# Performance work log

Hardware: AMD Instinct MI355X
Metric: run time of the kernel (lower is better)

The kernel has to match this reference:

```python
import jax, jax.numpy as jnp
import numpy as np

ALPHA = 0.2  # leaky relu slope
NEG = -9e15  # mask fill value from the torch code


def gat_layer(x, adj_mask, W, a):
    """One dense GAT attention head.
    Equivalent math to the torch layer, without materializing the
    [N, N, 2F] a_input tensor: a^T [h_i ; h_j] = (h @ a1)_i + (h @ a2)_j.
    x: [N, Fin], adj_mask: [N, N] bool, W: [Fin, Fout], a: [2*Fout, 1].
    """
    h = x @ W                              # [N, Fout]
    Fo = W.shape[1]
    s_src = h @ a[:Fo, 0]                  # [N]
    s_dst = h @ a[Fo:, 0]                  # [N]
    e = jax.nn.leaky_relu(s_src[:, None] + s_dst[None, :], ALPHA)  # [N, N]
    e = jnp.where(adj_mask, e, NEG)
    attn = jax.nn.softmax(e, axis=1)       # dropout is a no-op in eval mode
    return attn @ h                        # [N, Fout]


def setup_inputs() -> dict:
    key = jax.random.key(0)
    ks = jax.random.split(key, 6)
    N, nfeat, nhid, nclass, nheads = 4096, 512, 64, 32, 8
    x = jax.random.normal(ks[0], (N, nfeat), dtype=jnp.float32)
    adj = jax.random.randint(ks[1], (N, N), 0, 2, dtype=jnp.int32)
    # params scaled like torch uniform(-1/sqrt(fan_in), 1/sqrt(fan_in))
    W_att = jax.random.normal(ks[2], (nheads, nfeat, nhid), dtype=jnp.float32) / np.sqrt(nfeat)
    a_att = jax.random.normal(ks[3], (nheads, 2 * nhid, 1), dtype=jnp.float32) / np.sqrt(2 * nhid)
    W_out = jax.random.normal(ks[4], (nhid * nheads, nclass), dtype=jnp.float32) / np.sqrt(nhid * nheads)
    a_out = jax.random.normal(ks[5], (2 * nclass, 1), dtype=jnp.float32) / np.sqrt(2 * nclass)
    return {"x": x, "adj": adj, "W_att": W_att, "a_att": a_att,
            "W_out": W_out, "a_out": a_out}


def reference(x, adj, W_att, a_att, W_out, a_out):
    adj_mask = adj > 0  # [N, N]
    # multi-head layer, concat=True => elu per head, concat along features
    heads = jax.vmap(lambda W, a: jax.nn.elu(gat_layer(x, adj_mask, W, a)))(W_att, a_att)  # [H, N, nhid]
    H, N, Fh = heads.shape
    hcat = jnp.transpose(heads, (1, 0, 2)).reshape(N, H * Fh)  # [N, H*nhid]
    # output layer, concat=False, then elu applied by GAT.forward
    out = jax.nn.elu(gat_layer(hcat, adj_mask, W_out, a_out))  # [N, nclass]
    return out
```

## Files before the change

### kernel.cpp

```cpp
#include <hip/hip_runtime.h>
#include <math.h>

#define NN 4096
#define CC 512
#define MB (1024*1024)
#define LOG2E 1.4426950408889634f

typedef __attribute__((ext_vector_type(8))) __bf16 bf16x8;
typedef __attribute__((ext_vector_type(4))) float f32x4;
typedef unsigned short ushort_t;
typedef unsigned int uint_t;
typedef unsigned char uchar_t;

#if __has_builtin(__builtin_amdgcn_exp2f)
#define EXP2(x) __builtin_amdgcn_exp2f(x)
#else
#define EXP2(x) exp2f(x)
#endif

static __device__ __forceinline__ float elu1(float x){ return x > 0.f ? x : (__expf(x)-1.f); }
static __device__ __forceinline__ ushort_t f2bf(float f){
    union { float f; uint_t u; } v; v.f = f;
    uint_t r = (v.u + 0x7FFFu + ((v.u >> 16) & 1u)) >> 16;
    return (ushort_t)r;
}
static __device__ __forceinline__ float bf2f(ushort_t h){
    union { uint_t u; float f; } q; q.u = ((uint_t)h) << 16; return q.f;
}

__global__ void k_prep(const float* __restrict__ Watt, const float* __restrict__ Wout,
                       ushort_t* __restrict__ Wh, ushort_t* __restrict__ Wl,
                       ushort_t* __restrict__ Wth, ushort_t* __restrict__ Wtl){
    int idx = blockIdx.x*256 + threadIdx.x;
    if (idx < 512*128){
        int c = idx >> 7, kq = idx & 127, k = kq*4;
        ushort4 h4, l4;
        float v[4];
        #pragma unroll
        for(int j=0;j<4;j++)
            v[j] = Watt[(c>>6)*(512*64) + (k+j)*64 + (c&63)];
        h4.x = f2bf(v[0]); h4.y = f2bf(v[1]); h4.z = f2bf(v[2]); h4.w = f2bf(v[3]);
        l4.x = f2bf(v[0]-bf2f(h4.x)); l4.y = f2bf(v[1]-bf2f(h4.y));
        l4.z = f2bf(v[2]-bf2f(h4.z)); l4.w = f2bf(v[3]-bf2f(h4.w));
        *(ushort4*)&Wh[(size_t)c*512 + k] = h4;
        *(ushort4*)&Wl[(size_t)c*512 + k] = l4;
    } else if (idx < 512*128 + 32*128){
        int idx2 = idx - 512*128;
        int n = idx2 >> 7, kq = idx2 & 127, k = kq*4;
        ushort4 h4, l4;
        float v[4];
        #pragma unroll
        for(int j=0;j<4;j++)
            v[j] = Wout[(size_t)(k+j)*32 + n];
        h4.x = f2bf(v[0]); h4.y = f2bf(v[1]); h4.z = f2bf(v[2]); h4.w = f2bf(v[3]);
        l4.x = f2bf(v[0]-bf2f(h4.x)); l4.y = f2bf(v[1]-bf2f(h4.y));
        l4.z = f2bf(v[2]-bf2f(h4.z)); l4.w = f2bf(v[3]-bf2f(h4.w));
        *(ushort4*)&Wth[(size_t)n*512 + k] = h4;
        *(ushort4*)&Wtl[(size_t)n*512 + k] = l4;
    }
}

__global__ void k_splitx(const float* __restrict__ x,
                         ushort_t* __restrict__ xh, ushort_t* __restrict__ xl){
    int idx = blockIdx.x*256 + threadIdx.x;
    float4 v = *(const float4*)&x[(size_t)idx*4];
    ushort4 h4, l4;
    h4.x = f2bf(v.x); h4.y = f2bf(v.y); h4.z = f2bf(v.z); h4.w = f2bf(v.w);
    l4.x = f2bf(v.x-bf2f(h4.x)); l4.y = f2bf(v.y-bf2f(h4.y));
    l4.z = f2bf(v.z-bf2f(h4.z)); l4.w = f2bf(v.w-bf2f(h4.w));
    *(ushort4*)&xh[(size_t)idx*4] = h4;
    *(ushort4*)&xl[(size_t)idx*4] = l4;
}

__global__ void k_pack(const int* __restrict__ adj, uint_t* __restrict__ abits){
    int idx = blockIdx.x*256 + threadIdx.x;
    int i = idx >> 7, q = idx & 127;
    const int4* p = (const int4*)&adj[(size_t)i*NN + q*32];
    uint_t m = 0;
    #pragma unroll
    for(int g=0; g<8; g++){
        int4 v = p[g];
        m |= (uint_t)(v.x > 0) << (g*4 + 0);
        m |= (uint_t)(v.y > 0) << (g*4 + 1);
        m |= (uint_t)(v.z > 0) << (g*4 + 2);
        m |= (uint_t)(v.w > 0) << (g*4 + 3);
    }
    abits[idx] = m;
}

__global__ __launch_bounds__(256) void k_gemm1(
        const ushort_t* __restrict__ xh, const ushort_t* __restrict__ xl,
        const ushort_t* __restrict__ Wh, const ushort_t* __restrict__ Wl,
        const float* __restrict__ aatt,
        ushort_t* __restrict__ hT,
        float* __restrict__ ssrc2, float* __restrict__ sdst2){
    const int t = threadIdx.x;
    const int l = t & 63, wv = t >> 6;
    const int lr = l & 15, lg = l >> 4;
    const int ib = blockIdx.x*64 + wv*16;
    const int hd = blockIdx.y;
    const int j0 = hd*64;

    f32x4 acc[4] = {};
    #pragma unroll 2
    for(int ks=0; ks<16; ks++){
        const int kb = ks*32 + lg*8;
        bf16x8 ah = *(const bf16x8*)&xh[(size_t)(ib+lr)*512 + kb];
        bf16x8 al = *(const bf16x8*)&xl[(size_t)(ib+lr)*512 + kb];
        bf16x8 bh[4], bl[4];
        #pragma unroll
        for(int nt=0;nt<4;nt++){
            bh[nt] = *(const bf16x8*)&Wh[(size_t)(j0+nt*16+lr)*512 + kb];
            bl[nt] = *(const bf16x8*)&Wl[(size_t)(j0+nt*16+lr)*512 + kb];
        }
        #pragma unroll
        for(int nt=0;nt<4;nt++){
            acc[nt] = __builtin_amdgcn_mfma_f32_16x16x32_bf16(ah, bh[nt], acc[nt], 0,0,0);
            acc[nt] = __builtin_amdgcn_mfma_f32_16x16x32_bf16(al, bh[nt], acc[nt], 0,0,0);
            acc[nt] = __builtin_amdgcn_mfma_f32_16x16x32_bf16(ah, bl[nt], acc[nt], 0,0,0);
        }
    }
    #pragma unroll
    for(int nt=0;nt<4;nt++){
        const int col = j0 + nt*16 + lr;
        ushort4 o;
        o.x = f2bf(acc[nt][0]); o.y = f2bf(acc[nt][1]);
        o.z = f2bf(acc[nt][2]); o.w = f2bf(acc[nt][3]);
        *(ushort4*)&hT[(size_t)col*NN + ib + lg*4] = o;
    }
    float a1v[4], a2v[4];
    #pragma unroll
    for(int nt=0;nt<4;nt++){
        a1v[nt] = aatt[hd*128 + nt*16 + lr];
        a2v[nt] = aatt[hd*128 + 64 + nt*16 + lr];
    }
    #pragma unroll
    for(int r=0;r<4;r++){
        float ps = acc[0][r]*a1v[0] + acc[1][r]*a1v[1] + acc[2][r]*a1v[2] + acc[3][r]*a1v[3];
        float pd = acc[0][r]*a2v[0] + acc[1][r]*a2v[1] + acc[2][r]*a2v[2] + acc[3][r]*a2v[3];
        #pragma unroll
        for(int m=1;m<16;m<<=1){
            ps += __shfl_xor(ps, m);
            pd += __shfl_xor(pd, m);
        }
        if (lr == 0){
            ssrc2[hd*NN + ib + lg*4 + r] = ps*LOG2E;
            sdst2[hd*NN + ib + lg*4 + r] = pd*LOG2E;
        }
    }
}

__global__ __launch_bounds__(512, 2) void k_attn1(
        const ushort_t* __restrict__ hT,
        const float* __restrict__ ssrc2, const float* __restrict__ sdst2,
        const uchar_t* __restrict__ abits,
        ushort_t* __restrict__ hch, ushort_t* __restrict__ hcl){
    const int t = threadIdx.x;
    const int l = t & 63, wv = t >> 6;
    const int hd = blockIdx.y;
    const int i0 = blockIdx.x*64;
    const int lr = l & 15, lg = l >> 4;

    f32x4 acc[4][4] = {};
    f32x4 dacc[4] = {};

    float ss[4];
    #pragma unroll
    for(int mh=0;mh<4;mh++)
        ss[mh] = ssrc2[hd*NN + i0 + mh*16 + lr];

    bf16x8 ones;
    #pragma unroll
    for(int e=0;e<8;e++) ones[e] = (__bf16)1.0f;

    const int jwb = wv*512;
    const uchar_t* arow[4];
    #pragma unroll
    for(int mh=0;mh<4;mh++)
        arow[mh] = &abits[(size_t)(i0 + mh*16 + lr)*512 + (jwb >> 3)];

    bf16x8 bA[4], bB[4];
    float4 sdaA, sdbA, sdaB, sdbB;
    uint_t bitsA[4], bitsB[4];

#define LOAD1(SFX, JT) { \
    const int jb_ = jwb + (JT)*32 + lg*8; \
    _Pragma("unroll") \
    for(int nt=0;nt<4;nt++) \
        b##SFX[nt] = *(const bf16x8*)&hT[(size_t)(hd*64 + nt*16 + lr)*NN + jb_]; \
    sda##SFX = *(const float4*)&sdst2[hd*NN + jb_]; \
    sdb##SFX = *(const float4*)&sdst2[hd*NN + jb_ + 4]; \
    _Pragma("unroll") \
    for(int mh=0;mh<4;mh++) \
        bits##SFX[mh] = arow[mh][(JT)*4 + lg]; }

#define COMP1(SFX) { \
    float sdv[8] = {sda##SFX.x, sda##SFX.y, sda##SFX.z, sda##SFX.w, \
                    sdb##SFX.x, sdb##SFX.y, sdb##SFX.z, sdb##SFX.w}; \
    _Pragma("unroll") \
    for(int mh=0;mh<4;mh++){ \
        const uint_t bits = bits##SFX[mh]; \
        bf16x8 a; \
        _Pragma("unroll") \
        for(int e=0;e<8;e++){ \
            float s_ = ss[mh] + sdv[e]; \
            float t_ = fmaxf(s_, 0.2f*s_); \
            float w_ = EXP2(t_) * (float)((bits >> e) & 1u); \
            a[e] = (__bf16)w_; \
        } \
        _Pragma("unroll") \
        for(int nt=0;nt<4;nt++) \
            acc[mh][nt] = __builtin_amdgcn_mfma_f32_16x16x32_bf16( \
                a, b##SFX[nt], acc[mh][nt], 0, 0, 0); \
        dacc[mh] = __builtin_amdgcn_mfma_f32_16x16x32_bf16( \
                a, ones, dacc[mh], 0, 0, 0); \
    } }

    LOAD1(A, 0);
    for(int jt=0; jt<16; jt+=2){
        LOAD1(B, jt+1);
        COMP1(A);
        if (jt + 2 < 16) LOAD1(A, jt+2);
        COMP1(B);
    }
#undef LOAD1
#undef COMP1

    __shared__ f32x4 red[4][10][64];

#define CHUNK_REDUCE(M0) { \
    __syncthreads(); \
    if (wv >= 4){ \
        _Pragma("unroll") \
        for(int m=0;m<2;m++){ \
            _Pragma("unroll") \
            for(int nt=0;nt<4;nt++) red[wv-4][m*4+nt][l] = acc[(M0)+m][nt]; \
            red[wv-4][8+m][l] = dacc[(M0)+m]; \
        } \
    } \
    __syncthreads(); \
    if (wv < 4){ \
        _Pragma("unroll") \
        for(int m=0;m<2;m++){ \
            _Pragma("unroll") \
            for(int nt=0;nt<4;nt++) acc[(M0)+m][nt] += red[wv][m*4+nt][l]; \
            dacc[(M0)+m] += red[wv][8+m][l]; \
        } \
    } \
    __syncthreads(); \
    if (wv == 2 || wv == 3){ \
        _Pragma("unroll") \
        for(int m=0;m<2;m++){ \
            _Pragma("unroll") \
            for(int nt=0;nt<4;nt++) red[wv-2][m*4+nt][l] = acc[(M0)+m][nt]; \
            red[wv-2][8+m][l] = dacc[(M0)+m]; \
        } \
    } \
    __syncthreads(); \
    if (wv < 2){ \
        _Pragma("unroll") \
        for(int m=0;m<2;m++){ \
            _Pragma("unroll") \
            for(int nt=0;nt<4;nt++) acc[(M0)+m][nt] += red[wv][m*4+nt][l]; \
            dacc[(M0)+m] += red[wv][8+m][l]; \
        } \
    } \
    __syncthreads(); \
    if (wv == 1){ \
        _Pragma("unroll") \
        for(int m=0;m<2;m++){ \
            _Pragma("unroll") \
            for(int nt=0;nt<4;nt++) red[0][m*4+nt][l] = acc[(M0)+m][nt]; \
            red[0][8+m][l] = dacc[(M0)+m]; \
        } \
    } \
    __syncthreads(); \
    if (wv == 0){ \
        _Pragma("unroll") \
        for(int m=0;m<2;m++){ \
            const int mh = (M0)+m; \
            _Pragma("unroll") \
            for(int nt=0;nt<4;nt++) acc[mh][nt] += red[0][m*4+nt][l]; \
            dacc[mh] += red[0][8+m][l]; \
            _Pragma("unroll") \
            for(int nt=0;nt<4;nt++){ \
                const int col = hd*64 + nt*16 + lr; \
                _Pragma("unroll") \
                for(int r=0;r<4;r++){ \
                    const int row = i0 + mh*16 + lg*4 + r; \
                    float v_ = elu1(acc[mh][nt][r] / dacc[mh][r]); \
                    ushort_t hi_ = f2bf(v_); \
                    hch[(size_t)row*512 + col] = hi_; \
                    hcl[(size_t)row*512 + col] = f2bf(v_ - bf2f(hi_)); \
                } \
            } \
        } \
    } }

    CHUNK_REDUCE(0);
    CHUNK_REDUCE(2);
#undef CHUNK_REDUCE
}

__global__ __launch_bounds__(256) void k_gemm2(
        const ushort_t* __restrict__ hch, const ushort_t* __restrict__ hcl,
        const ushort_t* __restrict__ Wth, const ushort_t* __restrict__ Wtl,
        const float* __restrict__ aout,
        ushort_t* __restrict__ h2T, float* __restrict__ ss2, float* __restrict__ sd2){
    const int t = threadIdx.x;
    const int l = t & 63, wv = t >> 6;
    const int lr = l & 15, lg = l >> 4;
    const int ib = blockIdx.x*64 + wv*16;

    f32x4 acc[2] = {};
    #pragma unroll 2
    for(int ks=0; ks<16; ks++){
        const int kb = ks*32 + lg*8;
        bf16x8 ah = *(const bf16x8*)&hch[(size_t)(ib+lr)*512 + kb];
        bf16x8 al = *(const bf16x8*)&hcl[(size_t)(ib+lr)*512 + kb];
        bf16x8 bh[2], bl[2];
        #pragma unroll
        for(int nt=0;nt<2;nt++){
            bh[nt] = *(const bf16x8*)&Wth[(size_t)(nt*16+lr)*512 + kb];
            bl[nt] = *(const bf16x8*)&Wtl[(size_t)(nt*16+lr)*512 + kb];
        }
        #pragma unroll
        for(int nt=0;nt<2;nt++){
            acc[nt] = __builtin_amdgcn_mfma_f32_16x16x32_bf16(ah, bh[nt], acc[nt], 0,0,0);
            acc[nt] = __builtin_amdgcn_mfma_f32_16x16x32_bf16(al, bh[nt], acc[nt], 0,0,0);
            acc[nt] = __builtin_amdgcn_mfma_f32_16x16x32_bf16(ah, bl[nt], acc[nt], 0,0,0);
        }
    }
    #pragma unroll
    for(int nt=0;nt<2;nt++)
        #pragma unroll
        for(int r=0;r<4;r++)
            h2T[(size_t)(nt*16+lr)*NN + ib + lg*4 + r] = f2bf(acc[nt][r]);
    float a1v[2], a2v[2];
    #pragma unroll
    for(int nt=0;nt<2;nt++){
        a1v[nt] = aout[nt*16 + lr];
        a2v[nt] = aout[32 + nt*16 + lr];
    }
    #pragma unroll
    for(int r=0;r<4;r++){
        float ps = acc[0][r]*a1v[0] + acc[1][r]*a1v[1];
        float pd = acc[0][r]*a2v[0] + acc[1][r]*a2v[1];
        #pragma unroll
        for(int m=1;m<16;m<<=1){
            ps += __shfl_xor(ps, m);
            pd += __shfl_xor(pd, m);
        }
        if (lr == 0){
            ss2[ib + lg*4 + r] = ps*LOG2E;
            sd2[ib + lg*4 + r] = pd*LOG2E;
        }
    }
}

__global__ __launch_bounds__(256) void k_attn2(
        const ushort_t* __restrict__ h2T,
        const float* __restrict__ ss2, const float* __restrict__ sd2,
        const uchar_t* __restrict__ abits,
        float* __restrict__ pnum2T, float* __restrict__ pden2){
    const int t = threadIdx.x;
    const int l = t & 63, wv = t >> 6;
    const int i0 = blockIdx.x*64;
    const int jc = blockIdx.y;
    const int lr = l & 15, lg = l >> 4;

    f32x4 acc[4][2] = {};
    f32x4 dacc[4] = {};

    float ss[4];
    #pragma unroll
    for(int mh=0;mh<4;mh++)
        ss[mh] = ss2[i0 + mh*16 + lr];

    bf16x8 ones;
    #pragma unroll
    for(int e=0;e<8;e++) ones[e] = (__bf16)1.0f;

    const int jwb = jc*512 + wv*128;
    const uchar_t* arow[4];
    #pragma unroll
    for(int mh=0;mh<4;mh++)
        arow[mh] = &abits[(size_t)(i0 + mh*16 + lr)*512 + (jwb >> 3)];

    bf16x8 bA[2], bB[2];
    float4 sdaA, sdbA, sdaB, sdbB;
    uint_t bitsA[4], bitsB[4];

#define LOAD2(SFX, JT) { \
    const int jb_ = jwb + (JT)*32 + lg*8; \
    _Pragma("unroll") \
    for(int nt=0;nt<2;nt++) \
        b##SFX[nt] = *(const bf16x8*)&h2T[(size_t)(nt*16 + lr)*NN + jb_]; \
    sda##SFX = *(const float4*)&sd2[jb_]; \
    sdb##SFX = *(const float4*)&sd2[jb_ + 4]; \
    _Pragma("unroll") \
    for(int mh=0;mh<4;mh++) \
        bits##SFX[mh] = arow[mh][(JT)*4 + lg]; }

#define COMP2(SFX) { \
    float sdv[8] = {sda##SFX.x, sda##SFX.y, sda##SFX.z, sda##SFX.w, \
                    sdb##SFX.x, sdb##SFX.y, sdb##SFX.z, sdb##SFX.w}; \
    _Pragma("unroll") \
    for(int mh=0;mh<4;mh++){ \
        const uint_t bits = bits##SFX[mh]; \
        bf16x8 a; \
        _Pragma("unroll") \
        for(int e=0;e<8;e++){ \
            float s_ = ss[mh] + sdv[e]; \
            float t_ = fmaxf(s_, 0.2f*s_); \
            float w_ = EXP2(t_) * (float)((bits >> e) & 1u); \
            a[e] = (__bf16)w_; \
        } \
        _Pragma("unroll") \
        for(int nt=0;nt<2;nt++) \
            acc[mh][nt] = __builtin_amdgcn_mfma_f32_16x16x32_bf16( \
                a, b##SFX[nt], acc[mh][nt], 0, 0, 0); \
        dacc[mh] = __builtin_amdgcn_mfma_f32_16x16x32_bf16( \
                a, ones, dacc[mh], 0, 0, 0); \
    } }

    LOAD2(A, 0);
    for(int jt=0; jt<4; jt+=2){
        LOAD2(B, jt+1);
        COMP2(A);
        if (jt + 2 < 4) LOAD2(A, jt+2);
        COMP2(B);
    }
#undef LOAD2
#undef COMP2

    __shared__ f32x4 red2[2][12][64];
    __syncthreads();
    if (wv >= 2){
        #pragma unroll
        for(int mh=0;mh<4;mh++){
            #pragma unroll
            for(int nt=0;nt<2;nt++) red2[wv-2][mh*2+nt][l] = acc[mh][nt];
            red2[wv-2][8+mh][l] = dacc[mh];
        }
    }
    __syncthreads();
    if (wv < 2){
        #pragma unroll
        for(int mh=0;mh<4;mh++){
            #pragma unroll
            for(int nt=0;nt<2;nt++) acc[mh][nt] += red2[wv][mh*2+nt][l];
            dacc[mh] += red2[wv][8+mh][l];
        }
    }
    __syncthreads();
    if (wv == 1){
        #pragma unroll
        for(int mh=0;mh<4;mh++){
            #pragma unroll
            for(int nt=0;nt<2;nt++) red2[0][mh*2+nt][l] = acc[mh][nt];
            red2[0][8+mh][l] = dacc[mh];
        }
    }
    __syncthreads();
    if (wv == 0){
        #pragma unroll
        for(int mh=0;mh<4;mh++){
            #pragma unroll
            for(int nt=0;nt<2;nt++){
                f32x4 v = acc[mh][nt] + red2[0][mh*2+nt][l];
                int col = nt*16 + lr;
                float4 o = {v[0], v[1], v[2], v[3]};
                *(float4*)&pnum2T[((size_t)jc*32 + col)*NN + i0 + mh*16 + lg*4] = o;
            }
            f32x4 d = dacc[mh] + red2[0][8+mh][l];
            if (lr == 0){
                #pragma unroll
                for(int r=0;r<4;r++)
                    pden2[(size_t)jc*NN + i0 + mh*16 + lg*4 + r] = d[r];
            }
        }
    }
}

__global__ void k_reduce2(const float* __restrict__ pnum2T, const float* __restrict__ pden2,
                          float* __restrict__ out){
    int idx = blockIdx.x*256 + threadIdx.x;
    int c = idx >> 10, i4 = (idx & 1023)*4;
    f32x4 s = {}, d = {};
    #pragma unroll
    for(int jc=0;jc<8;jc++){
        s += *(const f32x4*)&pnum2T[((size_t)jc*32 + c)*NN + i4];
        d += *(const f32x4*)&pden2[(size_t)jc*NN + i4];
    }
    #pragma unroll
    for(int r=0;r<4;r++)
        out[(size_t)(i4+r)*32 + c] = elu1(s[r]/d[r]);
}

extern "C" void kernel_launch(void* const* d_in, const int* in_sizes, int n_in,
                              void* d_out, int out_size, void* d_ws, size_t ws_size,
                              hipStream_t stream){
    const float* x    = (const float*)d_in[0];
    const int*   adj  = (const int*)  d_in[1];
    const float* Watt = (const float*)d_in[2];
    const float* aatt = (const float*)d_in[3];
    const float* Wout = (const float*)d_in[4];
    const float* aout = (const float*)d_in[5];
    float* out = (float*)d_out;
    char* ws = (char*)d_ws;

    ushort_t* hch   = (ushort_t*)(ws + (size_t) 0*MB);
    ushort_t* hcl   = (ushort_t*)(ws + (size_t) 4*MB);
    ushort_t* Whi   = (ushort_t*)(ws + (size_t) 8*MB);
    ushort_t* Wlo   = (ushort_t*)(ws + (size_t) 8*MB + 512*1024);
    float*    ssrc2 = (float*)   (ws + (size_t) 9*MB);
    float*    sdst2 = (float*)   (ws + (size_t)10*MB);
    ushort_t* hT    = (ushort_t*)(ws + (size_t)11*MB);
    uint_t*   abits = (uint_t*)  (ws + (size_t)15*MB);
    ushort_t* Wth   = (ushort_t*)(ws + (size_t)17*MB);
    ushort_t* Wtl   = (ushort_t*)(ws + (size_t)17*MB + 64*1024);
    float*    ss2   = (float*)   (ws + (size_t)18*MB);
    float*    sd2   = (float*)   (ws + (size_t)19*MB);
    ushort_t* h2T   = (ushort_t*)(ws + (size_t)20*MB);
    float*    pden2 = (float*)   (ws + (size_t)21*MB);
    float*    pnum2T= (float*)   (ws + (size_t)22*MB);
    ushort_t* xh    = (ushort_t*)(ws + (size_t)26*MB);
    ushort_t* xl    = (ushort_t*)(ws + (size_t)30*MB);
    if (ws_size < (size_t)40*MB) return;

    k_prep    <<<272, 256, 0, stream>>>(Watt, Wout, Whi, Wlo, Wth, Wtl);
    k_splitx  <<<2048, 256, 0, stream>>>(x, xh, xl);
    k_pack    <<<2048, 256, 0, stream>>>(adj, abits);
    k_gemm1   <<<dim3(64,8), 256, 0, stream>>>(xh, xl, Whi, Wlo, aatt, hT, ssrc2, sdst2);
    k_attn1   <<<dim3(64,8), 512, 0, stream>>>(hT, ssrc2, sdst2, (const uchar_t*)abits, hch, hcl);
    k_gemm2   <<<64, 256, 0, stream>>>(hch, hcl, Wth, Wtl, aout, h2T, ss2, sd2);
    k_attn2   <<<dim3(64,8), 256, 0, stream>>>(h2T, ss2, sd2, (const uchar_t*)abits, pnum2T, pden2);
    k_reduce2 <<<128, 256, 0, stream>>>(pnum2T, pden2, out);
}
```

Before: 257.8 us.

## Merge prep kernels into one launch and retile attention to 32-row blocks

The three preprocessing kernels (weight split, x split, adjacency bit packing) become a single launch that dispatches on block index, removing two kernel launches. The first-layer attention kernel moves from 64-row, 8-wave blocks to 32-row, 4-wave blocks over twice as many blocks. Each wave now covers 1024 columns instead of 512 and holds half the accumulators. The multi-stage shared-memory tree reduction becomes a single store, one barrier, and a four-way sum. This trades register pressure and reduction barriers for more blocks, and each block now reloads its hT tiles for only 32 rows.

```diff
diff --git a/kernel.cpp b/kernel.cpp
--- a/kernel.cpp
+++ b/kernel.cpp
@@ -28,64 +28,65 @@
     union { uint_t u; float f; } q; q.u = ((uint_t)h) << 16; return q.f;
 }
 
-__global__ void k_prep(const float* __restrict__ Watt, const float* __restrict__ Wout,
-                       ushort_t* __restrict__ Wh, ushort_t* __restrict__ Wl,
-                       ushort_t* __restrict__ Wth, ushort_t* __restrict__ Wtl){
-    int idx = blockIdx.x*256 + threadIdx.x;
-    if (idx < 512*128){
-        int c = idx >> 7, kq = idx & 127, k = kq*4;
+__global__ void k_prepare(const float* __restrict__ x, const int* __restrict__ adj,
+                          const float* __restrict__ Watt, const float* __restrict__ Wout,
+                          ushort_t* __restrict__ xh, ushort_t* __restrict__ xl,
+                          uint_t* __restrict__ abits,
+                          ushort_t* __restrict__ Wh, ushort_t* __restrict__ Wl,
+                          ushort_t* __restrict__ Wth, ushort_t* __restrict__ Wtl){
+    const int bid = blockIdx.x;
+    if (bid < 2048){
+        int idx = bid*256 + threadIdx.x;
+        float4 v = *(const float4*)&x[(size_t)idx*4];
         ushort4 h4, l4;
-        float v[4];
-        #pragma unroll
-        for(int j=0;j<4;j++)
-            v[j] = Watt[(c>>6)*(512*64) + (k+j)*64 + (c&63)];
-        h4.x = f2bf(v[0]); h4.y = f2bf(v[1]); h4.z = f2bf(v[2]); h4.w = f2bf(v[3]);
-        l4.x = f2bf(v[0]-bf2f(h4.x)); l4.y = f2bf(v[1]-bf2f(h4.y));
-        l4.z = f2bf(v[2]-bf2f(h4.z)); l4.w = f2bf(v[3]-bf2f(h4.w));
-        *(ushort4*)&Wh[(size_t)c*512 + k] = h4;
-        *(ushort4*)&Wl[(size_t)c*512 + k] = l4;
-    } else if (idx < 512*128 + 32*128){
-        int idx2 = idx - 512*128;
-        int n = idx2 >> 7, kq = idx2 & 127, k = kq*4;
-        ushort4 h4, l4;
-        float v[4];
-        #pragma unroll
-        for(int j=0;j<4;j++)
-            v[j] = Wout[(size_t)(k+j)*32 + n];
-        h4.x = f2bf(v[0]); h4.y = f2bf(v[1]); h4.z = f2bf(v[2]); h4.w = f2bf(v[3]);
-        l4.x = f2bf(v[0]-bf2f(h4.x)); l4.y = f2bf(v[1]-bf2f(h4.y));
-        l4.z = f2bf(v[2]-bf2f(h4.z)); l4.w = f2bf(v[3]-bf2f(h4.w));
-        *(ushort4*)&Wth[(size_t)n*512 + k] = h4;
-        *(ushort4*)&Wtl[(size_t)n*512 + k] = l4;
-    }
-}
-
-__global__ void k_splitx(const float* __restrict__ x,
-                         ushort_t* __restrict__ xh, ushort_t* __restrict__ xl){
-    int idx = blockIdx.x*256 + threadIdx.x;
-    float4 v = *(const float4*)&x[(size_t)idx*4];
-    ushort4 h4, l4;
-    h4.x = f2bf(v.x); h4.y = f2bf(v.y); h4.z = f2bf(v.z); h4.w = f2bf(v.w);
-    l4.x = f2bf(v.x-bf2f(h4.x)); l4.y = f2bf(v.y-bf2f(h4.y));
-    l4.z = f2bf(v.z-bf2f(h4.z)); l4.w = f2bf(v.w-bf2f(h4.w));
-    *(ushort4*)&xh[(size_t)idx*4] = h4;
-    *(ushort4*)&xl[(size_t)idx*4] = l4;
-}
-
-__global__ void k_pack(const int* __restrict__ adj, uint_t* __restrict__ abits){
-    int idx = blockIdx.x*256 + threadIdx.x;
-    int i = idx >> 7, q = idx & 127;
-    const int4* p = (const int4*)&adj[(size_t)i*NN + q*32];
-    uint_t m = 0;
-    #pragma unroll
-    for(int g=0; g<8; g++){
-        int4 v = p[g];
-        m |= (uint_t)(v.x > 0) << (g*4 + 0);
-        m |= (uint_t)(v.y > 0) << (g*4 + 1);
-        m |= (uint_t)(v.z > 0) << (g*4 + 2);
-        m |= (uint_t)(v.w > 0) << (g*4 + 3);
-    }
-    abits[idx] = m;
+        h4.x = f2bf(v.x); h4.y = f2bf(v.y); h4.z = f2bf(v.z); h4.w = f2bf(v.w);
+        l4.x = f2bf(v.x-bf2f(h4.x)); l4.y = f2bf(v.y-bf2f(h4.y));
+        l4.z = f2bf(v.z-bf2f(h4.z)); l4.w = f2bf(v.w-bf2f(h4.w));
+        *(ushort4*)&xh[(size_t)idx*4] = h4;
+        *(ushort4*)&xl[(size_t)idx*4] = l4;
+    } else if (bid < 4096){
+        int idx = (bid-2048)*256 + threadIdx.x;
+        int i = idx >> 7, q = idx & 127;
+        const int4* p = (const int4*)&adj[(size_t)i*NN + q*32];
+        uint_t m = 0;
+        #pragma unroll
+        for(int g=0; g<8; g++){
+            int4 v = p[g];
+            m |= (uint_t)(v.x > 0) << (g*4 + 0);
+            m |= (uint_t)(v.y > 0) << (g*4 + 1);
+            m |= (uint_t)(v.z > 0) << (g*4 + 2);
+            m |= (uint_t)(v.w > 0) << (g*4 + 3);
+        }
+        abits[idx] = m;
+    } else {
+        int idx = (bid-4096)*256 + threadIdx.x;
+        if (idx < 512*128){
+            int c = idx >> 7, k = (idx & 127)*4;
+            ushort4 h4, l4;
+            float v[4];
+            #pragma unroll
+            for(int j=0;j<4;j++)
+                v[j] = Watt[(c>>6)*(512*64) + (k+j)*64 + (c&63)];
+            h4.x = f2bf(v[0]); h4.y = f2bf(v[1]); h4.z = f2bf(v[2]); h4.w = f2bf(v[3]);
+            l4.x = f2bf(v[0]-bf2f(h4.x)); l4.y = f2bf(v[1]-bf2f(h4.y));
+            l4.z = f2bf(v[2]-bf2f(h4.z)); l4.w = f2bf(v[3]-bf2f(h4.w));
+            *(ushort4*)&Wh[(size_t)c*512 + k] = h4;
+            *(ushort4*)&Wl[(size_t)c*512 + k] = l4;
+        } else if (idx < 512*128 + 32*128){
+            int idx2 = idx - 512*128;
+            int n = idx2 >> 7, k = (idx2 & 127)*4;
+            ushort4 h4, l4;
+            float v[4];
+            #pragma unroll
+            for(int j=0;j<4;j++)
+                v[j] = Wout[(size_t)(k+j)*32 + n];
+            h4.x = f2bf(v[0]); h4.y = f2bf(v[1]); h4.z = f2bf(v[2]); h4.w = f2bf(v[3]);
+            l4.x = f2bf(v[0]-bf2f(h4.x)); l4.y = f2bf(v[1]-bf2f(h4.y));
+            l4.z = f2bf(v[2]-bf2f(h4.z)); l4.w = f2bf(v[3]-bf2f(h4.w));
+            *(ushort4*)&Wth[(size_t)n*512 + k] = h4;
+            *(ushort4*)&Wtl[(size_t)n*512 + k] = l4;
+        }
+    }
 }
 
 __global__ __launch_bounds__(256) void k_gemm1(
@@ -150,7 +151,7 @@
     }
 }
 
-__global__ __launch_bounds__(512, 2) void k_attn1(
+__global__ __launch_bounds__(256) void k_attn1(
         const ushort_t* __restrict__ hT,
         const float* __restrict__ ssrc2, const float* __restrict__ sdst2,
         const uchar_t* __restrict__ abits,
@@ -158,30 +159,30 @@
     const int t = threadIdx.x;
     const int l = t & 63, wv = t >> 6;
     const int hd = blockIdx.y;
-    const int i0 = blockIdx.x*64;
+    const int i0 = blockIdx.x*32;
     const int lr = l & 15, lg = l >> 4;
 
-    f32x4 acc[4][4] = {};
-    f32x4 dacc[4] = {};
-
-    float ss[4];
-    #pragma unroll
-    for(int mh=0;mh<4;mh++)
+    f32x4 acc[2][4] = {};
+    f32x4 dacc[2] = {};
+
+    float ss[2];
+    #pragma unroll
+    for(int mh=0;mh<2;mh++)
         ss[mh] = ssrc2[hd*NN + i0 + mh*16 + lr];
 
     bf16x8 ones;
     #pragma unroll
     for(int e=0;e<8;e++) ones[e] = (__bf16)1.0f;
 
-    const int jwb = wv*512;
-    const uchar_t* arow[4];
-    #pragma unroll
-    for(int mh=0;mh<4;mh++)
+    const int jwb = wv*1024;
+    const uchar_t* arow[2];
+    #pragma unroll
+    for(int mh=0;mh<2;mh++)
         arow[mh] = &abits[(size_t)(i0 + mh*16 + lr)*512 + (jwb >> 3)];
 
     bf16x8 bA[4], bB[4];
     float4 sdaA, sdbA, sdaB, sdbB;
-    uint_t bitsA[4], bitsB[4];
+    uint_t bitsA[2], bitsB[2];
 
 #define LOAD1(SFX, JT) { \
     const int jb_ = jwb + (JT)*32 + lg*8; \
@@ -191,14 +192,14 @@
     sda##SFX = *(const float4*)&sdst2[hd*NN + jb_]; \
     sdb##SFX = *(const float4*)&sdst2[hd*NN + jb_ + 4]; \
     _Pragma("unroll") \
-    for(int mh=0;mh<4;mh++) \
+    for(int mh=0;mh<2;mh++) \
         bits##SFX[mh] = arow[mh][(JT)*4 + lg]; }
 
 #define COMP1(SFX) { \
     float sdv[8] = {sda##SFX.x, sda##SFX.y, sda##SFX.z, sda##SFX.w, \
                     sdb##SFX.x, sdb##SFX.y, sdb##SFX.z, sdb##SFX.w}; \
     _Pragma("unroll") \
-    for(int mh=0;mh<4;mh++){ \
+    for(int mh=0;mh<2;mh++){ \
         const uint_t bits = bits##SFX[mh]; \
         bf16x8 a; \
         _Pragma("unroll") \
@@ -217,89 +218,45 @@
     } }
 
     LOAD1(A, 0);
-    for(int jt=0; jt<16; jt+=2){
+    for(int jt=0; jt<32; jt+=2){
         LOAD1(B, jt+1);
         COMP1(A);
-        if (jt + 2 < 16) LOAD1(A, jt+2);
+        if (jt + 2 < 32) LOAD1(A, jt+2);
         COMP1(B);
     }
 #undef LOAD1
 #undef COMP1
 
     __shared__ f32x4 red[4][10][64];
-
-#define CHUNK_REDUCE(M0) { \
-    __syncthreads(); \
-    if (wv >= 4){ \
-        _Pragma("unroll") \
-        for(int m=0;m<2;m++){ \
-            _Pragma("unroll") \
-            for(int nt=0;nt<4;nt++) red[wv-4][m*4+nt][l] = acc[(M0)+m][nt]; \
-            red[wv-4][8+m][l] = dacc[(M0)+m]; \
-        } \
-    } \
-    __syncthreads(); \
-    if (wv < 4){ \
-        _Pragma("unroll") \
-        for(int m=0;m<2;m++){ \
-            _Pragma("unroll") \
-            for(int nt=0;nt<4;nt++) acc[(M0)+m][nt] += red[wv][m*4+nt][l]; \
-            dacc[(M0)+m] += red[wv][8+m][l]; \
-        } \
-    } \
-    __syncthreads(); \
-    if (wv == 2 || wv == 3){ \
-        _Pragma("unroll") \
-        for(int m=0;m<2;m++){ \
-            _Pragma("unroll") \
-            for(int nt=0;nt<4;nt++) red[wv-2][m*4+nt][l] = acc[(M0)+m][nt]; \
-            red[wv-2][8+m][l] = dacc[(M0)+m]; \
-        } \
-    } \
-    __syncthreads(); \
-    if (wv < 2){ \
-        _Pragma("unroll") \
-        for(int m=0;m<2;m++){ \
-            _Pragma("unroll") \
-            for(int nt=0;nt<4;nt++) acc[(M0)+m][nt] += red[wv][m*4+nt][l]; \
-            dacc[(M0)+m] += red[wv][8+m][l]; \
-        } \
-    } \
-    __syncthreads(); \
-    if (wv == 1){ \
-        _Pragma("unroll") \
-        for(int m=0;m<2;m++){ \
-            _Pragma("unroll") \
-            for(int nt=0;nt<4;nt++) red[0][m*4+nt][l] = acc[(M0)+m][nt]; \
-            red[0][8+m][l] = dacc[(M0)+m]; \
-        } \
-    } \
-    __syncthreads(); \
-    if (wv == 0){ \
-        _Pragma("unroll") \
-        for(int m=0;m<2;m++){ \
-            const int mh = (M0)+m; \
-            _Pragma("unroll") \
-            for(int nt=0;nt<4;nt++) acc[mh][nt] += red[0][m*4+nt][l]; \
-            dacc[mh] += red[0][8+m][l]; \
-            _Pragma("unroll") \
-            for(int nt=0;nt<4;nt++){ \
-                const int col = hd*64 + nt*16 + lr; \
-                _Pragma("unroll") \
-                for(int r=0;r<4;r++){ \
-                    const int row = i0 + mh*16 + lg*4 + r; \
-                    float v_ = elu1(acc[mh][nt][r] / dacc[mh][r]); \
-                    ushort_t hi_ = f2bf(v_); \
-                    hch[(size_t)row*512 + col] = hi_; \
-                    hcl[(size_t)row*512 + col] = f2bf(v_ - bf2f(hi_)); \
-                } \
-            } \
-        } \
-    } }
-
-    CHUNK_REDUCE(0);
-    CHUNK_REDUCE(2);
-#undef CHUNK_REDUCE
+    #pragma unroll
+    for(int mh=0;mh<2;mh++){
+        #pragma unroll
+        for(int nt=0;nt<4;nt++) red[wv][mh*5+nt][l] = acc[mh][nt];
+        red[wv][mh*5+4][l] = dacc[mh];
+    }
+    __syncthreads();
+    if (wv < 2){
+        const int mh = wv;
+        f32x4 s[4], dd;
+        #pragma unroll
+        for(int nt=0;nt<4;nt++)
+            s[nt] = red[0][mh*5+nt][l] + red[1][mh*5+nt][l]
+                  + red[2][mh*5+nt][l] + red[3][mh*5+nt][l];
+        dd = red[0][mh*5+4][l] + red[1][mh*5+4][l]
+           + red[2][mh*5+4][l] + red[3][mh*5+4][l];
+        #pragma unroll
+        for(int nt=0;nt<4;nt++){
+            const int col = hd*64 + nt*16 + lr;
+            #pragma unroll
+            for(int r=0;r<4;r++){
+                const int row = i0 + mh*16 + lg*4 + r;
+                float v_ = elu1(s[nt][r] / dd[r]);
+                ushort_t hi_ = f2bf(v_);
+                hch[(size_t)row*512 + col] = hi_;
+                hcl[(size_t)row*512 + col] = f2bf(v_ - bf2f(hi_));
+            }
+        }
+    }
 }
 
 __global__ __launch_bounds__(256) void k_gemm2(
@@ -529,11 +486,10 @@
     ushort_t* xl    = (ushort_t*)(ws + (size_t)30*MB);
     if (ws_size < (size_t)40*MB) return;
 
-    k_prep    <<<272, 256, 0, stream>>>(Watt, Wout, Whi, Wlo, Wth, Wtl);
-    k_splitx  <<<2048, 256, 0, stream>>>(x, xh, xl);
-    k_pack    <<<2048, 256, 0, stream>>>(adj, abits);
+    k_prepare <<<4368, 256, 0, stream>>>(x, adj, Watt, Wout, xh, xl, abits,
+                                         Whi, Wlo, Wth, Wtl);
     k_gemm1   <<<dim3(64,8), 256, 0, stream>>>(xh, xl, Whi, Wlo, aatt, hT, ssrc2, sdst2);
-    k_attn1   <<<dim3(64,8), 512, 0, stream>>>(hT, ssrc2, sdst2, (const uchar_t*)abits, hch, hcl);
+    k_attn1   <<<dim3(128,8), 256, 0, stream>>>(hT, ssrc2, sdst2, (const uchar_t*)abits, hch, hcl);
     k_gemm2   <<<64, 256, 0, stream>>>(hch, hcl, Wth, Wtl, aout, h2T, ss2, sd2);
     k_attn2   <<<dim3(64,8), 256, 0, stream>>>(h2T, ss2, sd2, (const uchar_t*)abits, pnum2T, pden2);
     k_reduce2 <<<128, 256, 0, stream>>>(pnum2T, pden2, out);
```

After: 273.4 us. +6.1%, slower.
